# Kernel optimization log

Measured on AMD Instinct MI355X. Metric: run time of the kernel, lower is better.

## Reference

```python
import jax, jax.numpy as jnp
import numpy as np

T, N, E = 8, 100000, 1600000
D_IN, D_H, D_E = 64, 64, 16
FLAT = D_IN * D_H            # 4096
BNECK = max(FLAT // 4, 32)   # 1024


def setup_inputs() -> dict:
    key = jax.random.key(0)
    ks = jax.random.split(key, 12)
    return {
        "x_seq": jax.random.normal(ks[0], (T, N, D_IN), dtype=jnp.float32),
        "edge_attr": jax.random.normal(ks[1], (E, D_E), dtype=jnp.float32),
        "init_w": jax.random.normal(ks[2], (D_IN, D_H), dtype=jnp.float32) * 0.1,   # ~xavier scale
        "ode_w1": jax.random.normal(ks[3], (FLAT, BNECK), dtype=jnp.float32) * 0.02,
        "ode_b1": jax.random.normal(ks[4], (BNECK,), dtype=jnp.float32) * 0.02,
        "ode_w2": jax.random.normal(ks[5], (BNECK, FLAT), dtype=jnp.float32) * 0.02,
        "ode_b2": jax.random.normal(ks[6], (FLAT,), dtype=jnp.float32) * 0.02,
        "mlp_w1": jax.random.normal(ks[7], (2 * D_H + D_E, D_H), dtype=jnp.float32) * 0.08,
        "mlp_b1": jax.random.normal(ks[8], (D_H,), dtype=jnp.float32) * 0.02,
        "mlp_w2": jax.random.normal(ks[9], (D_H, 1), dtype=jnp.float32) * 0.1,
        "mlp_b2": jax.random.normal(ks[10], (1,), dtype=jnp.float32) * 0.02,
        "edge_index": jax.random.randint(ks[11], (2, E), 0, N, dtype=jnp.int32),
    }


def _forward(x_seq, edge_attr, init_w, ode_w1, ode_b1, ode_w2, ode_b2,
             mlp_w1, mlp_b1, mlp_w2, mlp_b2, edge_index):
    n_t, n_nodes, d_in = x_seq.shape

    # --- Weight ODE: dW/dt = MLP(W), torchdiffeq fixed-step 'rk4' (3/8-rule alt step),
    # step_size = 1/(T-1) so each interval of linspace(0,1,T) is exactly one step.
    def f(w):
        return jnp.tanh(w @ ode_w1 + ode_b1) @ ode_w2 + ode_b2

    h = 1.0 / (n_t - 1)

    def rk4_alt_step(w, _):
        k1 = f(w)
        k2 = f(w + h * k1 / 3.0)
        k3 = f(w + h * (k2 - k1 / 3.0))
        k4 = f(w + h * (k1 - k2 + k3))
        w_next = w + h * (k1 + 3.0 * (k2 + k3) + k4) * 0.125
        return w_next, None

    w0 = init_w.reshape(-1)                                   # [FLAT]
    w_last, _ = jax.lax.scan(rk4_alt_step, w0, None, length=n_t - 1)
    W_T = w_last.reshape(d_in, -1)                            # [D_IN, D_H]

    # --- GCN on the last graph (intermediate timestep embeddings are discarded
    # by the original loop, so only W[T-1] and x_seq[-1] affect the output).
    row, col = edge_index[0], edge_index[1]
    ar = jnp.arange(n_nodes, dtype=edge_index.dtype)
    row_l = jnp.concatenate([row, ar])                        # self-loops appended
    col_l = jnp.concatenate([col, ar])

    deg = jax.ops.segment_sum(jnp.ones_like(col_l, dtype=x_seq.dtype), col_l,
                              num_segments=n_nodes)
    dis = jnp.where(deg > 0, jax.lax.rsqrt(jnp.maximum(deg, 1e-12)), 0.0)
    norm = dis[row_l] * dis[col_l]                            # [E+N]

    xw = x_seq[-1] @ W_T                                      # [N, D_H]
    msg = norm[:, None] * xw[row_l]                           # gather
    h_nodes = jax.ops.segment_sum(msg, col_l, num_segments=n_nodes)  # scatter-add
    h_nodes = jax.nn.relu(h_nodes)                            # dropout = identity (eval)

    # --- Edge MLP on original edges of the last graph
    edge_in = jnp.concatenate([h_nodes[row], h_nodes[col], edge_attr], axis=1)  # [E, 2H+F]
    hid = jax.nn.relu(edge_in @ mlp_w1 + mlp_b1)
    out = (hid @ mlp_w2 + mlp_b2).squeeze(-1)                 # [E]
    return out


def reference(x_seq, edge_attr, init_w, ode_w1, ode_b1, ode_w2, ode_b2,
              mlp_w1, mlp_b1, mlp_w2, mlp_b2, edge_index):
    return _forward(x_seq, edge_attr, init_w, ode_w1, ode_b1, ode_w2, ode_b2,
                    mlp_w1, mlp_b1, mlp_w2, mlp_b2, edge_index)
```

## Files before the change

kernel.cpp:

```cpp
#include <hip/hip_runtime.h>
#include <cstddef>

#define NT   8
#define NN   100000
#define NE   1600000
#define DIN  64
#define DH   64
#define DE   16
#define FLAT 4096
#define BN   1024

__device__ __forceinline__ void atomAdd(float* p, float v) { unsafeAtomicAdd(p, v); }

__device__ __forceinline__ void fma4(float4& a, float s, const float4& w) {
  a.x = fmaf(s, w.x, a.x); a.y = fmaf(s, w.y, a.y);
  a.z = fmaf(s, w.z, a.z); a.w = fmaf(s, w.w, a.w);
}

__global__ void k_init(const float* __restrict__ init_w, float* __restrict__ wbuf,
                       float* __restrict__ kbuf, float* __restrict__ acc1,
                       int* __restrict__ cnt) {
  int i = blockIdx.x * blockDim.x + threadIdx.x;
  if (i < FLAT) wbuf[FLAT + i] = init_w[i];
  if (i < 8 * FLAT) kbuf[i] = 0.f;
  if (i < 2 * BN) acc1[i] = 0.f;
  for (int n = i; n < NN; n += gridDim.x * blockDim.x) cnt[n] = 0;
}

__global__ __launch_bounds__(256) void k_odeA(
    const float* __restrict__ w1, const float* __restrict__ wbase,
    const float* __restrict__ kbase, float c0, float c1, float c2, float c3,
    float* __restrict__ acc_dst, float* __restrict__ acc_zero,
    float* __restrict__ k_zero, float* __restrict__ w_store) {
  __shared__ float win[256];
  __shared__ float red[256];
  const int t = threadIdx.x;
  const int ic = blockIdx.x & 15, jc = blockIdx.x >> 4;
  const int i0 = ic * 256;
  if (t < 16) k_zero[blockIdx.x * 16 + t] = 0.f;
  if (t >= 16 && t < 20) acc_zero[blockIdx.x * 4 + (t - 16)] = 0.f;
  {
    int i = i0 + t;
    float v = wbase[i] + c0 * kbase[i] + c1 * kbase[FLAT + i]
            + c2 * kbase[2 * FLAT + i] + c3 * kbase[3 * FLAT + i];
    win[t] = v;
    if (w_store != nullptr && jc == 0) w_store[i] = v;
  }
  __syncthreads();
  const int jl = t & 63, ig = t >> 6;
  const int j = jc * 64 + jl;
  const float* wp = w1 + (size_t)(i0 + ig * 64) * BN + j;
  float acc = 0.f;
#pragma unroll 8
  for (int ii = 0; ii < 64; ++ii)
    acc = fmaf(win[ig * 64 + ii], wp[(size_t)ii * BN], acc);
  red[t] = acc;
  __syncthreads();
  if (t < 64) {
    float s = red[t] + red[t + 64] + red[t + 128] + red[t + 192];
    atomAdd(&acc_dst[jc * 64 + t], s);
  }
}

__global__ __launch_bounds__(256) void k_odeB(
    const float* __restrict__ w2, const float* __restrict__ acc_src,
    const float* __restrict__ b1, const float* __restrict__ b2,
    float* __restrict__ k_dst) {
  __shared__ float tl[64];
  const int t = threadIdx.x;
  const int ic = blockIdx.x & 15, jc = blockIdx.x >> 4;
  const int i0 = ic * 64;
  if (t < 64) tl[t] = tanhf(acc_src[i0 + t] + b1[i0 + t]);
  __syncthreads();
  const int j = jc * 256 + t;
  const float* wp = w2 + (size_t)i0 * FLAT + j;
  float acc = (ic == 0) ? b2[j] : 0.f;
#pragma unroll 8
  for (int ii = 0; ii < 64; ++ii)
    acc = fmaf(tl[ii], wp[(size_t)ii * FLAT], acc);
  atomAdd(&k_dst[j], acc);
}

__global__ void k_final(const float* __restrict__ w0, const float* __restrict__ k0,
                        float* __restrict__ WT) {
  int i = blockIdx.x * blockDim.x + threadIdx.x;
  if (i < FLAT) {
    const float h8 = (1.0f / 7.0f) * 0.125f;
    WT[i] = w0[i] + h8 * (k0[i] + 3.f * (k0[FLAT + i] + k0[2 * FLAT + i]) + k0[3 * FLAT + i]);
  }
}

__global__ void k_hist(const int* __restrict__ ei, int* __restrict__ cnt) {
  int e = blockIdx.x * blockDim.x + threadIdx.x;
  if (e < NE) atomicAdd(&cnt[ei[NE + e]], 1);
}

__global__ __launch_bounds__(256) void k_scan1(const int* __restrict__ cnt,
                                               int* __restrict__ offs,
                                               int* __restrict__ bsum) {
  __shared__ int s[256];
  const int t = threadIdx.x;
  const int i = blockIdx.x * 256 + t;
  int v = (i < NN) ? cnt[i] : 0;
  s[t] = v;
  __syncthreads();
  for (int off = 1; off < 256; off <<= 1) {
    int x = (t >= off) ? s[t - off] : 0;
    __syncthreads();
    s[t] += x;
    __syncthreads();
  }
  if (i < NN) offs[i] = s[t] - v;
  if (t == 255) bsum[blockIdx.x] = s[255];
}

__global__ __launch_bounds__(512) void k_scan2(int* __restrict__ bsum,
                                               int* __restrict__ bofs, int nblk) {
  __shared__ int s[512];
  const int t = threadIdx.x;
  int v = (t < nblk) ? bsum[t] : 0;
  s[t] = v;
  __syncthreads();
  for (int off = 1; off < 512; off <<= 1) {
    int x = (t >= off) ? s[t - off] : 0;
    __syncthreads();
    s[t] += x;
    __syncthreads();
  }
  if (t < nblk) bofs[t] = s[t] - v;
}

__global__ __launch_bounds__(256) void k_scan3(const int* __restrict__ cnt,
                                               int* __restrict__ offs,
                                               const int* __restrict__ bofs,
                                               int* __restrict__ cur,
                                               float* __restrict__ dis) {
  const int i = blockIdx.x * 256 + threadIdx.x;
  if (i < NN) {
    int o = offs[i] + bofs[i >> 8];
    offs[i] = o;
    cur[i] = o;
    dis[i] = rsqrtf((float)(cnt[i] + 1));
  }
  if (i == 0) offs[NN] = NE;
}

__global__ void k_fill(const int* __restrict__ ei, int* __restrict__ cur,
                       int2* __restrict__ csr) {
  int e = blockIdx.x * blockDim.x + threadIdx.x;
  if (e < NE) {
    int row = ei[e], col = ei[NE + e];
    int pos = atomicAdd(&cur[col], 1);
    csr[pos] = make_int2(row, e);
  }
}

__global__ __launch_bounds__(256) void k_xw(
    const float* __restrict__ x_last, const float* __restrict__ WT,
    float* __restrict__ xw) {
  __shared__ float wt[FLAT];
  for (int i = threadIdx.x; i < FLAT; i += 256) wt[i] = WT[i];
  __syncthreads();
  const int lane = threadIdx.x & 15;
  const int grp = threadIdx.x >> 4;
  const int n0 = blockIdx.x * 64 + grp * 4;
  if (n0 >= NN) return;
  const int nvalid = (NN - n0 < 4) ? (NN - n0) : 4;
  const float4* xp[4];
#pragma unroll
  for (int m = 0; m < 4; ++m) {
    int n = (m < nvalid) ? (n0 + m) : n0;
    xp[m] = (const float4*)(x_last + (size_t)n * 64);
  }
  float4 acc[4];
#pragma unroll
  for (int m = 0; m < 4; ++m) acc[m] = make_float4(0.f, 0.f, 0.f, 0.f);
#pragma unroll
  for (int q = 0; q < 16; ++q) {
    const float* wr = &wt[(q * 4) * 64 + lane * 4];
    float4 w0 = *(const float4*)&wr[0];
    float4 w1 = *(const float4*)&wr[64];
    float4 w2 = *(const float4*)&wr[128];
    float4 w3 = *(const float4*)&wr[192];
#pragma unroll
    for (int m = 0; m < 4; ++m) {
      float4 x4 = xp[m][q];
      fma4(acc[m], x4.x, w0); fma4(acc[m], x4.y, w1);
      fma4(acc[m], x4.z, w2); fma4(acc[m], x4.w, w3);
    }
  }
  for (int m = 0; m < nvalid; ++m)
    *(float4*)&xw[(size_t)(n0 + m) * 64 + lane * 4] = acc[m];
}

__global__ __launch_bounds__(256) void k_gh(
    const int* __restrict__ offs, const int2* __restrict__ csr,
    const float* __restrict__ dis, const float* __restrict__ xw,
    float* __restrict__ h) {
  const int node = blockIdx.x * 4 + (threadIdx.x >> 6);
  const int lane = threadIdx.x & 63;
  if (node >= NN) return;
  const int off0 = offs[node], off1 = offs[node + 1];
  const float d = dis[node];
  float acc = d * d * xw[(size_t)node * 64 + lane];
  int e = off0;
  for (; e + 3 < off1; e += 4) {
    int2 c0 = csr[e], c1 = csr[e + 1], c2 = csr[e + 2], c3 = csr[e + 3];
    float x0 = xw[(size_t)c0.x * 64 + lane];
    float x1 = xw[(size_t)c1.x * 64 + lane];
    float x2 = xw[(size_t)c2.x * 64 + lane];
    float x3 = xw[(size_t)c3.x * 64 + lane];
    float n0 = d * dis[c0.x], n1 = d * dis[c1.x];
    float n2 = d * dis[c2.x], n3 = d * dis[c3.x];
    acc = fmaf(n0, x0, acc);
    acc = fmaf(n1, x1, acc);
    acc = fmaf(n2, x2, acc);
    acc = fmaf(n3, x3, acc);
  }
  for (; e < off1; ++e) {
    int2 c0 = csr[e];
    acc = fmaf(d * dis[c0.x], xw[(size_t)c0.x * 64 + lane], acc);
  }
  h[(size_t)node * 64 + lane] = fmaxf(acc, 0.f);
}

__global__ __launch_bounds__(256) void k_finalize(
    const float* __restrict__ mlp_w1, const float* __restrict__ mlp_b1,
    float* __restrict__ hA, float* __restrict__ Bb) {
  __shared__ float wa[FLAT];
  __shared__ float wb[FLAT];
  for (int i = threadIdx.x; i < FLAT; i += 256) {
    wa[i] = mlp_w1[i];
    wb[i] = mlp_w1[FLAT + i];
  }
  __syncthreads();
  const int lane = threadIdx.x & 15;
  const int grp = threadIdx.x >> 4;
  const int n0 = blockIdx.x * 64 + grp * 4;
  if (n0 >= NN) return;
  const int nvalid = (NN - n0 < 4) ? (NN - n0) : 4;
  const float4 b1v = ((const float4*)mlp_b1)[lane];
  const float4* hp[4];
#pragma unroll
  for (int m = 0; m < 4; ++m) {
    int n = (m < nvalid) ? (n0 + m) : n0;
    hp[m] = (const float4*)(hA + (size_t)n * 64);
  }
  float4 aA[4], aB[4];
#pragma unroll
  for (int m = 0; m < 4; ++m) { aA[m] = make_float4(0,0,0,0); aB[m] = make_float4(0,0,0,0); }
#pragma unroll
  for (int q = 0; q < 16; ++q) {
    const float* war = &wa[(q * 4) * 64 + lane * 4];
    const float* wbr = &wb[(q * 4) * 64 + lane * 4];
    float4 wa0 = *(const float4*)&war[0];
    float4 wa1 = *(const float4*)&war[64];
    float4 wa2 = *(const float4*)&war[128];
    float4 wa3 = *(const float4*)&war[192];
    float4 wb0 = *(const float4*)&wbr[0];
    float4 wb1 = *(const float4*)&wbr[64];
    float4 wb2 = *(const float4*)&wbr[128];
    float4 wb3 = *(const float4*)&wbr[192];
#pragma unroll
    for (int m = 0; m < 4; ++m) {
      float4 h4 = hp[m][q];
      fma4(aA[m], h4.x, wa0); fma4(aA[m], h4.y, wa1); fma4(aA[m], h4.z, wa2); fma4(aA[m], h4.w, wa3);
      fma4(aB[m], h4.x, wb0); fma4(aB[m], h4.y, wb1); fma4(aB[m], h4.z, wb2); fma4(aB[m], h4.w, wb3);
    }
  }
  for (int m = 0; m < nvalid; ++m) {
    *(float4*)&hA[(size_t)(n0 + m) * 64 + lane * 4] = aA[m];
    float4 bo = aB[m];
    bo.x += b1v.x; bo.y += b1v.y; bo.z += b1v.z; bo.w += b1v.w;
    *(float4*)&Bb[(size_t)(n0 + m) * 64 + lane * 4] = bo;
  }
}

__global__ __launch_bounds__(256) void k_emlp(
    const int* __restrict__ ei, const float* __restrict__ A,
    const float* __restrict__ Bb, const float* __restrict__ eattr,
    const float* __restrict__ mlp_w1, const float* __restrict__ mlp_w2,
    const float* __restrict__ mlp_b2, float* __restrict__ out) {
  const int lane = threadIdx.x & 63;
  const int e0 = __builtin_amdgcn_readfirstlane((blockIdx.x * 4 + (threadIdx.x >> 6)) * 8);
  if (e0 >= NE) return;
  float wc[16];
#pragma unroll
  for (int f = 0; f < 16; ++f) wc[f] = mlp_w1[(size_t)(128 + f) * 64 + lane];
  const float w2l = mlp_w2[lane];
  const float b2v = mlp_b2[0];
  const int4 r01 = *(const int4*)&ei[e0];
  const int4 r23 = *(const int4*)&ei[e0 + 4];
  const int4 c01 = *(const int4*)&ei[NE + e0];
  const int4 c23 = *(const int4*)&ei[NE + e0 + 4];
  const float av0 = A[(size_t)r01.x * 64 + lane], bv0 = Bb[(size_t)c01.x * 64 + lane];
  const float av1 = A[(size_t)r01.y * 64 + lane], bv1 = Bb[(size_t)c01.y * 64 + lane];
  const float av2 = A[(size_t)r01.z * 64 + lane], bv2 = Bb[(size_t)c01.z * 64 + lane];
  const float av3 = A[(size_t)r01.w * 64 + lane], bv3 = Bb[(size_t)c01.w * 64 + lane];
  const float av4 = A[(size_t)r23.x * 64 + lane], bv4 = Bb[(size_t)c23.x * 64 + lane];
  const float av5 = A[(size_t)r23.y * 64 + lane], bv5 = Bb[(size_t)c23.y * 64 + lane];
  const float av6 = A[(size_t)r23.z * 64 + lane], bv6 = Bb[(size_t)c23.z * 64 + lane];
  const float av7 = A[(size_t)r23.w * 64 + lane], bv7 = Bb[(size_t)c23.w * 64 + lane];
  const float4* ep = (const float4*)(eattr + (size_t)e0 * 16);

#define EDOT(acc, Ea, Eb, Ec, Ed)                                    \
  acc = fmaf(Ea.x, wc[0], acc);  acc = fmaf(Ea.y, wc[1], acc);       \
  acc = fmaf(Ea.z, wc[2], acc);  acc = fmaf(Ea.w, wc[3], acc);       \
  acc = fmaf(Eb.x, wc[4], acc);  acc = fmaf(Eb.y, wc[5], acc);       \
  acc = fmaf(Eb.z, wc[6], acc);  acc = fmaf(Eb.w, wc[7], acc);       \
  acc = fmaf(Ec.x, wc[8], acc);  acc = fmaf(Ec.y, wc[9], acc);       \
  acc = fmaf(Ec.z, wc[10], acc); acc = fmaf(Ec.w, wc[11], acc);      \
  acc = fmaf(Ed.x, wc[12], acc); acc = fmaf(Ed.y, wc[13], acc);      \
  acc = fmaf(Ed.z, wc[14], acc); acc = fmaf(Ed.w, wc[15], acc)

  float p0, p1, p2, p3, p4, p5, p6, p7;
  {
    float4 E00 = ep[0],  E01 = ep[1],  E02 = ep[2],  E03 = ep[3];
    float4 E10 = ep[4],  E11 = ep[5],  E12 = ep[6],  E13 = ep[7];
    float4 E20 = ep[8],  E21 = ep[9],  E22 = ep[10], E23 = ep[11];
    float4 E30 = ep[12], E31 = ep[13], E32 = ep[14], E33 = ep[15];
    p0 = av0 + bv0; EDOT(p0, E00, E01, E02, E03); p0 = fmaxf(p0, 0.f) * w2l;
    p1 = av1 + bv1; EDOT(p1, E10, E11, E12, E13); p1 = fmaxf(p1, 0.f) * w2l;
    p2 = av2 + bv2; EDOT(p2, E20, E21, E22, E23); p2 = fmaxf(p2, 0.f) * w2l;
    p3 = av3 + bv3; EDOT(p3, E30, E31, E32, E33); p3 = fmaxf(p3, 0.f) * w2l;
  }
  {
    float4 E00 = ep[16], E01 = ep[17], E02 = ep[18], E03 = ep[19];
    float4 E10 = ep[20], E11 = ep[21], E12 = ep[22], E13 = ep[23];
    float4 E20 = ep[24], E21 = ep[25], E22 = ep[26], E23 = ep[27];
    float4 E30 = ep[28], E31 = ep[29], E32 = ep[30], E33 = ep[31];
    p4 = av4 + bv4; EDOT(p4, E00, E01, E02, E03); p4 = fmaxf(p4, 0.f) * w2l;
    p5 = av5 + bv5; EDOT(p5, E10, E11, E12, E13); p5 = fmaxf(p5, 0.f) * w2l;
    p6 = av6 + bv6; EDOT(p6, E20, E21, E22, E23); p6 = fmaxf(p6, 0.f) * w2l;
    p7 = av7 + bv7; EDOT(p7, E30, E31, E32, E33); p7 = fmaxf(p7, 0.f) * w2l;
  }
#undef EDOT

  p0 += __shfl_xor(p0, 1); p1 += __shfl_xor(p1, 1);
  p2 += __shfl_xor(p2, 1); p3 += __shfl_xor(p3, 1);
  p4 += __shfl_xor(p4, 1); p5 += __shfl_xor(p5, 1);
  p6 += __shfl_xor(p6, 1); p7 += __shfl_xor(p7, 1);
  float u0 = (lane & 1) ? p1 : p0;
  float u1 = (lane & 1) ? p3 : p2;
  float u2 = (lane & 1) ? p5 : p4;
  float u3 = (lane & 1) ? p7 : p6;
  u0 += __shfl_xor(u0, 2); u1 += __shfl_xor(u1, 2);
  u2 += __shfl_xor(u2, 2); u3 += __shfl_xor(u3, 2);
  float v0 = (lane & 2) ? u1 : u0;
  float v1 = (lane & 2) ? u3 : u2;
  v0 += __shfl_xor(v0, 4); v1 += __shfl_xor(v1, 4);
  float s = (lane & 4) ? v1 : v0;
  s += __shfl_xor(s, 8);
  s += __shfl_xor(s, 16);
  s += __shfl_xor(s, 32);
  if (lane < 8) out[e0 + lane] = s + b2v;
}

extern "C" void kernel_launch(void* const* d_in, const int* in_sizes, int n_in,
                              void* d_out, int out_size, void* d_ws, size_t ws_size,
                              hipStream_t stream) {
  (void)in_sizes; (void)n_in; (void)out_size; (void)ws_size;
  const float* x_seq  = (const float*)d_in[0];
  const float* eattr  = (const float*)d_in[1];
  const float* init_w = (const float*)d_in[2];
  const float* ode_w1 = (const float*)d_in[3];
  const float* ode_b1 = (const float*)d_in[4];
  const float* ode_w2 = (const float*)d_in[5];
  const float* ode_b2 = (const float*)d_in[6];
  const float* mlp_w1 = (const float*)d_in[7];
  const float* mlp_b1 = (const float*)d_in[8];
  const float* mlp_w2 = (const float*)d_in[9];
  const float* mlp_b2 = (const float*)d_in[10];
  const int*   eidx   = (const int*)d_in[11];
  float* out = (float*)d_out;

  float* ws   = (float*)d_ws;
  float* wbuf = ws;
  float* kbuf = wbuf + 2 * FLAT;
  float* acc1 = kbuf + 8 * FLAT;
  float* WT   = acc1 + 2 * BN;
  float* dis  = ws + 49152;
  int*   cnt  = (int*)(ws + 149152);
  int*   offs = (int*)(ws + 249152);
  int*   bsum = (int*)(ws + 349184);
  int*   bofs = (int*)(ws + 349696);
  int*   cur  = (int*)(ws + 350208);
  int2*  csr  = (int2*)(ws + 450560);
  float* xw   = ws + 450560 + 2 * (size_t)NE;
  float* hA   = xw + (size_t)NN * 64;

  const int nblk_n = (NN + 255) / 256;

  k_init<<<128, 256, 0, stream>>>(init_w, wbuf, kbuf, acc1, cnt);
  k_hist<<<(NE + 255) / 256, 256, 0, stream>>>(eidx, cnt);
  k_scan1<<<nblk_n, 256, 0, stream>>>(cnt, offs, bsum);
  k_scan2<<<1, 512, 0, stream>>>(bsum, bofs, nblk_n);
  k_scan3<<<nblk_n, 256, 0, stream>>>(cnt, offs, bofs, cur, dis);
  k_fill<<<(NE + 255) / 256, 256, 0, stream>>>(eidx, cur, csr);

  const float h = 1.0f / 7.0f;
  for (int s = 0; s < 7; ++s) {
    int p = s & 1;
    for (int c = 0; c < 4; ++c) {
      int ev = s * 4 + c, pe = ev & 1;
      float c0, c1, c2, c3;
      const float* wb;
      float* wst = nullptr;
      int kp;
      if (c == 0) {
        c0 = h * 0.125f; c1 = 3.f * h * 0.125f; c2 = c1; c3 = c0;
        wb = wbuf + (1 - p) * FLAT; kp = 1 - p; wst = wbuf + p * FLAT;
      } else if (c == 1) {
        c0 = h / 3.f; c1 = 0.f; c2 = 0.f; c3 = 0.f; wb = wbuf + p * FLAT; kp = p;
      } else if (c == 2) {
        c0 = -h / 3.f; c1 = h; c2 = 0.f; c3 = 0.f; wb = wbuf + p * FLAT; kp = p;
      } else {
        c0 = h; c1 = -h; c2 = h; c3 = 0.f; wb = wbuf + p * FLAT; kp = p;
      }
      k_odeA<<<256, 256, 0, stream>>>(ode_w1, wb, kbuf + (size_t)kp * 4 * FLAT,
                                      c0, c1, c2, c3,
                                      acc1 + pe * BN, acc1 + (1 - pe) * BN,
                                      kbuf + (size_t)(p * 4 + c) * FLAT, wst);
      k_odeB<<<256, 256, 0, stream>>>(ode_w2, acc1 + pe * BN, ode_b1, ode_b2,
                                      kbuf + (size_t)(p * 4 + c) * FLAT);
    }
  }
  k_final<<<16, 256, 0, stream>>>(wbuf, kbuf, WT);

  k_xw<<<(NN + 63) / 64, 256, 0, stream>>>(x_seq + (size_t)(NT - 1) * NN * DIN, WT, xw);
  k_gh<<<(NN + 3) / 4, 256, 0, stream>>>(offs, csr, dis, xw, hA);
  k_finalize<<<(NN + 63) / 64, 256, 0, stream>>>(mlp_w1, mlp_b1, hA, xw);
  k_emlp<<<NE / 32, 256, 0, stream>>>(eidx, hA, xw, eattr,
                                      mlp_w1, mlp_w2, mlp_b2, out);
}
```

Baseline: 1.146 ms.

## Fuse RK4 weight-ODE into one persistent cooperative kernel with LDS-resident weights

The 56 separate odeA/odeB launches, plus the init and final kernels, become one cooperative kernel of 256 blocks. Each block loads its slice of ode_w1 and ode_w2 into shared memory once and keeps it there for all 28 function evaluations. Blocks exchange the hidden pre-activations and the updated W through global memory, separated by grid-wide syncs, and the RK4 stage combination is computed in registers. This removes repeated weight streaming and per-launch overhead, but adds two grid.sync barriers per stage and needs about 150KB of LDS per block, which relies on all 256 blocks being co-resident.

```diff
diff --git a/kernel.cpp b/kernel.cpp
--- a/kernel.cpp
+++ b/kernel.cpp
@@ -1,5 +1,8 @@
 #include <hip/hip_runtime.h>
+#include <hip/hip_cooperative_groups.h>
 #include <cstddef>
+
+namespace cg = cooperative_groups;
 
 #define NT   8
 #define NN   100000
@@ -17,77 +20,93 @@
   a.z = fmaf(s, w.z, a.z); a.w = fmaf(s, w.w, a.w);
 }
 
-__global__ void k_init(const float* __restrict__ init_w, float* __restrict__ wbuf,
-                       float* __restrict__ kbuf, float* __restrict__ acc1,
-                       int* __restrict__ cnt) {
+__global__ void k_init(int* __restrict__ cnt) {
   int i = blockIdx.x * blockDim.x + threadIdx.x;
-  if (i < FLAT) wbuf[FLAT + i] = init_w[i];
-  if (i < 8 * FLAT) kbuf[i] = 0.f;
-  if (i < 2 * BN) acc1[i] = 0.f;
   for (int n = i; n < NN; n += gridDim.x * blockDim.x) cnt[n] = 0;
 }
 
-__global__ __launch_bounds__(256) void k_odeA(
-    const float* __restrict__ w1, const float* __restrict__ wbase,
-    const float* __restrict__ kbase, float c0, float c1, float c2, float c3,
-    float* __restrict__ acc_dst, float* __restrict__ acc_zero,
-    float* __restrict__ k_zero, float* __restrict__ w_store) {
-  __shared__ float win[256];
+__global__ __launch_bounds__(256) void k_ode(
+    const float* __restrict__ init_w, const float* __restrict__ w1g,
+    const float* __restrict__ b1g, const float* __restrict__ w2g,
+    const float* __restrict__ b2g, float* __restrict__ win_g,
+    float* __restrict__ accg, float* __restrict__ WT) {
+  __shared__ float w1s[4][FLAT];
+  __shared__ float w2s[BN][16];
+  __shared__ float win_l[FLAT];
+  __shared__ float tl[BN];
+  __shared__ float b1s[BN];
   __shared__ float red[256];
-  const int t = threadIdx.x;
-  const int ic = blockIdx.x & 15, jc = blockIdx.x >> 4;
-  const int i0 = ic * 256;
-  if (t < 16) k_zero[blockIdx.x * 16 + t] = 0.f;
-  if (t >= 16 && t < 20) acc_zero[blockIdx.x * 4 + (t - 16)] = 0.f;
-  {
-    int i = i0 + t;
-    float v = wbase[i] + c0 * kbase[i] + c1 * kbase[FLAT + i]
-            + c2 * kbase[2 * FLAT + i] + c3 * kbase[3 * FLAT + i];
-    win[t] = v;
-    if (w_store != nullptr && jc == 0) w_store[i] = v;
-  }
+  __shared__ float wloc[16], b2loc[16], karr[4][16];
+  cg::grid_group grid = cg::this_grid();
+  const int t = threadIdx.x, b = blockIdx.x;
+  const int lane = t & 63, wv = t >> 6;
+
+  for (int i = t; i < FLAT; i += 256) {
+    float4 v = *(const float4*)&w1g[(size_t)i * BN + b * 4];
+    w1s[0][i] = v.x; w1s[1][i] = v.y; w1s[2][i] = v.z; w1s[3][i] = v.w;
+  }
+  for (int q = t; q < BN * 4; q += 256) {
+    int j = q >> 2, qq = (q & 3) * 4;
+    float4 v = *(const float4*)&w2g[(size_t)j * FLAT + b * 16 + qq];
+    w2s[j][qq] = v.x; w2s[j][qq + 1] = v.y; w2s[j][qq + 2] = v.z; w2s[j][qq + 3] = v.w;
+  }
+  for (int q = t; q < BN; q += 256) b1s[q] = b1g[q];
+  if (t < 16) { wloc[t] = init_w[b * 16 + t]; b2loc[t] = b2g[b * 16 + t]; }
   __syncthreads();
-  const int jl = t & 63, ig = t >> 6;
-  const int j = jc * 64 + jl;
-  const float* wp = w1 + (size_t)(i0 + ig * 64) * BN + j;
-  float acc = 0.f;
+
+  const float hh = 1.0f / 7.0f;
+  for (int s = 0; s < 7; ++s) {
+    for (int c = 0; c < 4; ++c) {
+      const float* wsrc = (s == 0 && c == 0) ? init_w : win_g;
+      for (int q = t; q < BN; q += 256)
+        *(float4*)&win_l[q * 4] = *(const float4*)&wsrc[q * 4];
+      __syncthreads();
+      float acc = 0.f;
 #pragma unroll 8
-  for (int ii = 0; ii < 64; ++ii)
-    acc = fmaf(win[ig * 64 + ii], wp[(size_t)ii * BN], acc);
-  red[t] = acc;
-  __syncthreads();
-  if (t < 64) {
-    float s = red[t] + red[t + 64] + red[t + 128] + red[t + 192];
-    atomAdd(&acc_dst[jc * 64 + t], s);
-  }
-}
-
-__global__ __launch_bounds__(256) void k_odeB(
-    const float* __restrict__ w2, const float* __restrict__ acc_src,
-    const float* __restrict__ b1, const float* __restrict__ b2,
-    float* __restrict__ k_dst) {
-  __shared__ float tl[64];
-  const int t = threadIdx.x;
-  const int ic = blockIdx.x & 15, jc = blockIdx.x >> 4;
-  const int i0 = ic * 64;
-  if (t < 64) tl[t] = tanhf(acc_src[i0 + t] + b1[i0 + t]);
-  __syncthreads();
-  const int j = jc * 256 + t;
-  const float* wp = w2 + (size_t)i0 * FLAT + j;
-  float acc = (ic == 0) ? b2[j] : 0.f;
+      for (int it = 0; it < 64; ++it) {
+        int i = it * 64 + lane;
+        acc = fmaf(win_l[i], w1s[wv][i], acc);
+      }
+      acc += __shfl_xor(acc, 1);
+      acc += __shfl_xor(acc, 2);
+      acc += __shfl_xor(acc, 4);
+      acc += __shfl_xor(acc, 8);
+      acc += __shfl_xor(acc, 16);
+      acc += __shfl_xor(acc, 32);
+      if (lane == 0) accg[b * 4 + wv] = acc;
+      __threadfence();
+      grid.sync();
+      for (int q = t; q < BN; q += 256) tl[q] = tanhf(accg[q] + b1s[q]);
+      __syncthreads();
+      const int ii = t & 15, jg = t >> 4;
+      float part = 0.f;
 #pragma unroll 8
-  for (int ii = 0; ii < 64; ++ii)
-    acc = fmaf(tl[ii], wp[(size_t)ii * FLAT], acc);
-  atomAdd(&k_dst[j], acc);
-}
-
-__global__ void k_final(const float* __restrict__ w0, const float* __restrict__ k0,
-                        float* __restrict__ WT) {
-  int i = blockIdx.x * blockDim.x + threadIdx.x;
-  if (i < FLAT) {
-    const float h8 = (1.0f / 7.0f) * 0.125f;
-    WT[i] = w0[i] + h8 * (k0[i] + 3.f * (k0[FLAT + i] + k0[2 * FLAT + i]) + k0[3 * FLAT + i]);
-  }
+      for (int jt = 0; jt < 64; ++jt) {
+        int j = jg * 64 + jt;
+        part = fmaf(tl[j], w2s[j][ii], part);
+      }
+      red[t] = part;
+      __syncthreads();
+      if (t < 16) {
+        float y = b2loc[t];
+#pragma unroll
+        for (int k = 0; k < 16; ++k) y += red[k * 16 + t];
+        karr[c][t] = y;
+        float wn;
+        if (c == 0)      wn = wloc[t] + hh * y * (1.f / 3.f);
+        else if (c == 1) wn = wloc[t] + hh * (y - karr[0][t] * (1.f / 3.f));
+        else if (c == 2) wn = wloc[t] + hh * (karr[0][t] - karr[1][t] + y);
+        else {
+          wn = wloc[t] + hh * 0.125f * (karr[0][t] + 3.f * (karr[1][t] + karr[2][t]) + y);
+          wloc[t] = wn;
+        }
+        win_g[b * 16 + t] = wn;
+      }
+      __threadfence();
+      grid.sync();
+    }
+  }
+  if (t < 16) WT[b * 16 + t] = wloc[t];
 }
 
 __global__ void k_hist(const int* __restrict__ ei, int* __restrict__ cnt) {
@@ -374,58 +393,35 @@
   const int*   eidx   = (const int*)d_in[11];
   float* out = (float*)d_out;
 
-  float* ws   = (float*)d_ws;
-  float* wbuf = ws;
-  float* kbuf = wbuf + 2 * FLAT;
-  float* acc1 = kbuf + 8 * FLAT;
-  float* WT   = acc1 + 2 * BN;
-  float* dis  = ws + 49152;
-  int*   cnt  = (int*)(ws + 149152);
-  int*   offs = (int*)(ws + 249152);
-  int*   bsum = (int*)(ws + 349184);
-  int*   bofs = (int*)(ws + 349696);
-  int*   cur  = (int*)(ws + 350208);
-  int2*  csr  = (int2*)(ws + 450560);
-  float* xw   = ws + 450560 + 2 * (size_t)NE;
-  float* hA   = xw + (size_t)NN * 64;
+  float* ws    = (float*)d_ws;
+  float* win_g = ws;
+  float* accg  = ws + 8 * FLAT;
+  float* WT    = ws + 10 * FLAT;
+  float* dis   = ws + 49152;
+  int*   cnt   = (int*)(ws + 149152);
+  int*   offs  = (int*)(ws + 249152);
+  int*   bsum  = (int*)(ws + 349184);
+  int*   bofs  = (int*)(ws + 349696);
+  int*   cur   = (int*)(ws + 350208);
+  int2*  csr   = (int2*)(ws + 450560);
+  float* xw    = ws + 450560 + 2 * (size_t)NE;
+  float* hA    = xw + (size_t)NN * 64;
 
   const int nblk_n = (NN + 255) / 256;
 
-  k_init<<<128, 256, 0, stream>>>(init_w, wbuf, kbuf, acc1, cnt);
+  k_init<<<128, 256, 0, stream>>>(cnt);
   k_hist<<<(NE + 255) / 256, 256, 0, stream>>>(eidx, cnt);
   k_scan1<<<nblk_n, 256, 0, stream>>>(cnt, offs, bsum);
   k_scan2<<<1, 512, 0, stream>>>(bsum, bofs, nblk_n);
   k_scan3<<<nblk_n, 256, 0, stream>>>(cnt, offs, bofs, cur, dis);
   k_fill<<<(NE + 255) / 256, 256, 0, stream>>>(eidx, cur, csr);
 
-  const float h = 1.0f / 7.0f;
-  for (int s = 0; s < 7; ++s) {
-    int p = s & 1;
-    for (int c = 0; c < 4; ++c) {
-      int ev = s * 4 + c, pe = ev & 1;
-      float c0, c1, c2, c3;
-      const float* wb;
-      float* wst = nullptr;
-      int kp;
-      if (c == 0) {
-        c0 = h * 0.125f; c1 = 3.f * h * 0.125f; c2 = c1; c3 = c0;
-        wb = wbuf + (1 - p) * FLAT; kp = 1 - p; wst = wbuf + p * FLAT;
-      } else if (c == 1) {
-        c0 = h / 3.f; c1 = 0.f; c2 = 0.f; c3 = 0.f; wb = wbuf + p * FLAT; kp = p;
-      } else if (c == 2) {
-        c0 = -h / 3.f; c1 = h; c2 = 0.f; c3 = 0.f; wb = wbuf + p * FLAT; kp = p;
-      } else {
-        c0 = h; c1 = -h; c2 = h; c3 = 0.f; wb = wbuf + p * FLAT; kp = p;
-      }
-      k_odeA<<<256, 256, 0, stream>>>(ode_w1, wb, kbuf + (size_t)kp * 4 * FLAT,
-                                      c0, c1, c2, c3,
-                                      acc1 + pe * BN, acc1 + (1 - pe) * BN,
-                                      kbuf + (size_t)(p * 4 + c) * FLAT, wst);
-      k_odeB<<<256, 256, 0, stream>>>(ode_w2, acc1 + pe * BN, ode_b1, ode_b2,
-                                      kbuf + (size_t)(p * 4 + c) * FLAT);
-    }
-  }
-  k_final<<<16, 256, 0, stream>>>(wbuf, kbuf, WT);
+  {
+    void* kargs[] = {(void*)&init_w, (void*)&ode_w1, (void*)&ode_b1,
+                     (void*)&ode_w2, (void*)&ode_b2, (void*)&win_g,
+                     (void*)&accg, (void*)&WT};
+    hipLaunchCooperativeKernel((void*)k_ode, dim3(256), dim3(256), kargs, 0, stream);
+  }
 
   k_xw<<<(NN + 63) / 64, 256, 0, stream>>>(x_seq + (size_t)(NT - 1) * NN * DIN, WT, xw);
   k_gh<<<(NN + 3) / 4, 256, 0, stream>>>(offs, csr, dis, xw, hA);
```

Result: slower. 3.640 ms (+217.6%).
